# Kernel optimization log

Hardware: AMD Instinct MI355X
Metric: run time of the kernel (lower is better)

The kernel has to match this reference:

```python
import jax, jax.numpy as jnp
import numpy as np

N, D = 262144, 64
L, K = 4, 1024


def setup_inputs() -> dict:
    key = jax.random.key(0)
    k1, k2 = jax.random.split(key)
    features = jax.random.normal(k1, (N, D), dtype=jnp.float32)
    codebooks = jax.random.normal(k2, (L, K, D), dtype=jnp.float32)
    return {"features": features, "codebooks": codebooks}


def reference(features, codebooks):
    """Residual VQ: per level, nearest-center (L2) argmin, gather, subtract.

    Uses squared distances (same argmin as torch.cdist p=2).
    """

    def step(residuals, centers):
        # ||r - c||^2 = ||r||^2 - 2 r.c + ||c||^2   -> [N, K]
        d = (
            jnp.sum(residuals * residuals, axis=1, keepdims=True)
            - 2.0 * (residuals @ centers.T)
            + jnp.sum(centers * centers, axis=1)
        )
        idx = jnp.argmin(d, axis=1)          # [N] int32
        quantized = centers[idx]             # [N, D] gather
        return residuals - quantized, (quantized, idx)

    _, (quantized_levels, indices) = jax.lax.scan(step, features, codebooks)
    quantized_result = jnp.sum(quantized_levels, axis=0)  # sum over L levels
    return quantized_result, indices  # indices: [L, N]
```

## Files before the change

### kernel.cpp

```cpp
#include <hip/hip_runtime.h>
#include <math.h>

constexpr int RVQ_N = 262144;
constexpr int RVQ_D = 64;
constexpr int RVQ_L = 4;
constexpr int RVQ_K = 1024;

typedef __attribute__((ext_vector_type(8))) short short8;
typedef __attribute__((ext_vector_type(4))) float floatx4;

__device__ __forceinline__ unsigned short f2bf(float f) {
  unsigned int u = __float_as_uint(f);
  u += 0x7fffu + ((u >> 16) & 1u);
  return (unsigned short)(u >> 16);
}
__device__ __forceinline__ float bf2f(unsigned short h) {
  return __uint_as_float(((unsigned int)h) << 16);
}
__device__ __forceinline__ void split2(float x, unsigned short& h0,
                                       unsigned short& h1) {
  h0 = f2bf(x);
  float r1 = x - bf2f(h0);
  h1 = f2bf(r1);
}
__device__ __forceinline__ void load8(const float* p, float* v) {
  float4 a = *(const float4*)p;
  float4 b = *(const float4*)(p + 4);
  v[0] = a.x; v[1] = a.y; v[2] = a.z; v[3] = a.w;
  v[4] = b.x; v[5] = b.y; v[6] = b.z; v[7] = b.w;
}

__device__ __forceinline__ unsigned med3u(unsigned a, unsigned b, unsigned c) {
  unsigned d;
  asm("v_med3_u32 %0, %1, %2, %3" : "=v"(d) : "v"(a), "v"(b), "v"(c));
  return d;
}

__device__ __forceinline__ unsigned rowmin16(unsigned x) {
  unsigned y;
  y = (unsigned)__builtin_amdgcn_update_dpp(0, (int)x, 0x121, 0xF, 0xF, true);
  x = x < y ? x : y;
  y = (unsigned)__builtin_amdgcn_update_dpp(0, (int)x, 0x122, 0xF, 0xF, true);
  x = x < y ? x : y;
  y = (unsigned)__builtin_amdgcn_update_dpp(0, (int)x, 0x124, 0xF, 0xF, true);
  x = x < y ? x : y;
  y = (unsigned)__builtin_amdgcn_update_dpp(0, (int)x, 0x128, 0xF, 0xF, true);
  x = x < y ? x : y;
  return x;
}

__global__ __launch_bounds__(256) void rvq_prep_split(
    const float* __restrict__ cb, unsigned short* __restrict__ bh,
    unsigned short* __restrict__ bm) {
  int i = blockIdx.x * 256 + threadIdx.x;
  float c2 = -2.0f * cb[i];
  unsigned short h0, h1;
  split2(c2, h0, h1);
  bh[i] = h0;
  bm[i] = h1;
}

__global__ __launch_bounds__(256) void rvq_cnorm_kernel(
    const float* __restrict__ cb, float* __restrict__ cnorm,
    float* __restrict__ cnormB) {
  int i = blockIdx.x * blockDim.x + threadIdx.x;
  const float* c = cb + (size_t)i * RVQ_D;
  float a0 = 0.f, a1 = 0.f, a2 = 0.f, a3 = 0.f;
#pragma unroll
  for (int d = 0; d < RVQ_D; d += 4) {
    float4 v = *reinterpret_cast<const float4*>(c + d);
    a0 = fmaf(v.x, v.x, a0);
    a1 = fmaf(v.y, v.y, a1);
    a2 = fmaf(v.z, v.z, a2);
    a3 = fmaf(v.w, v.w, a3);
  }
  float s = (a0 + a1) + (a2 + a3);
  cnorm[i] = s;
  cnormB[i] = s + 256.0f;
}

__device__ __forceinline__ void load_bt(const unsigned short* __restrict__ bh,
                                        const unsigned short* __restrict__ bmp,
                                        const float* __restrict__ cnl, int nt,
                                        int m, int q, short8 (&b)[2][2],
                                        float& cc) {
  size_t rowoff = (size_t)(nt * 16 + m) * RVQ_D + q * 8;
  b[0][0] = *(const short8*)(bh + rowoff);
  b[0][1] = *(const short8*)(bh + rowoff + 32);
  b[1][0] = *(const short8*)(bmp + rowoff);
  b[1][1] = *(const short8*)(bmp + rowoff + 32);
  cc = cnl[nt * 16 + m];
}

__global__ __launch_bounds__(64, 3) void rvq_mfma_kernel(
    const float* __restrict__ feat, const float* __restrict__ cb,
    const unsigned short* __restrict__ cb_hi,
    const unsigned short* __restrict__ cb_mid,
    const float* __restrict__ cnorm, const float* __restrict__ cnormB,
    float* __restrict__ out_q, float* __restrict__ out_idx) {
  const int lane = threadIdx.x & 63;
  const int m = lane & 15;
  const int q = lane >> 4;
  const int base = blockIdx.x * 64;
  const int g = base + lane;

  int ci0 = 0, ci1 = 0, ci2 = 0;

  constexpr int AC[3] = {0, 0, 1};
  constexpr int BC[3] = {0, 1, 0};

#pragma unroll 1
  for (int l = 0; l < RVQ_L; ++l) {
    const unsigned short* bh = cb_hi + (size_t)l * RVQ_K * RVQ_D;
    const unsigned short* bmp = cb_mid + (size_t)l * RVQ_K * RVQ_D;
    const float* cnBl = cnormB + (size_t)l * RVQ_K;
    const float* cnl = cnorm + (size_t)l * RVQ_K;
    const float* cbl = cb + (size_t)l * RVQ_K * RVQ_D;

    short8 afr[4][2][2];
#pragma unroll
    for (int t = 0; t < 4; ++t) {
      const int p = t * 16 + m;
      int j0 = 0, j1 = 0, j2 = 0;
      if (l > 0) j0 = __shfl(ci0, p);
      if (l > 1) j1 = __shfl(ci1, p);
      if (l > 2) j2 = __shfl(ci2, p);
      const float* fp = feat + (size_t)(base + p) * RVQ_D;
      const float* c0p = cb + (size_t)j0 * RVQ_D;
      const float* c1p = cb + ((size_t)RVQ_K + j1) * RVQ_D;
      const float* c2p = cb + ((size_t)2 * RVQ_K + j2) * RVQ_D;
#pragma unroll
      for (int oct = 0; oct < 2; ++oct) {
        const int dof = oct * 32 + q * 8;
        float v[8];
        load8(fp + dof, v);
        if (l > 0) {
          float c[8];
          load8(c0p + dof, c);
#pragma unroll
          for (int e = 0; e < 8; ++e) v[e] -= c[e];
        }
        if (l > 1) {
          float c[8];
          load8(c1p + dof, c);
#pragma unroll
          for (int e = 0; e < 8; ++e) v[e] -= c[e];
        }
        if (l > 2) {
          float c[8];
          load8(c2p + dof, c);
#pragma unroll
          for (int e = 0; e < 8; ++e) v[e] -= c[e];
        }
#pragma unroll
        for (int e = 0; e < 8; ++e) {
          unsigned short h0, h1;
          split2(v[e], h0, h1);
          afr[t][0][oct][e] = (short)h0;
          afr[t][1][oct][e] = (short)h1;
        }
      }
    }

    unsigned p1[4][4], p2[4][4];
#pragma unroll
    for (int t = 0; t < 4; ++t)
#pragma unroll
      for (int r2 = 0; r2 < 4; ++r2) {
        p1[t][r2] = 0xFFFFFFFFu;
        p2[t][r2] = 0xFFFFFFFFu;
      }

    short8 bA[2][2], bB[2][2];
    float ccA, ccB;
    load_bt(bh, bmp, cnBl, 0, m, q, bA, ccA);

    for (int nt = 0; nt < RVQ_K / 16; nt += 2) {
      load_bt(bh, bmp, cnBl, nt + 1, m, q, bB, ccB);
      {
        floatx4 ccv;
        ccv[0] = ccA; ccv[1] = ccA; ccv[2] = ccA; ccv[3] = ccA;
        floatx4 acc[4];
        __builtin_amdgcn_s_setprio(1);
#pragma unroll
        for (int t = 0; t < 4; ++t) {
          floatx4 a = __builtin_amdgcn_mfma_f32_16x16x32_bf16(
              afr[t][AC[0]][0], bA[BC[0]][0], ccv, 0, 0, 0);
#pragma unroll
          for (int s = 0; s < 3; ++s)
#pragma unroll
            for (int oct = 0; oct < 2; ++oct) {
              if (s == 0 && oct == 0) continue;
              a = __builtin_amdgcn_mfma_f32_16x16x32_bf16(
                  afr[t][AC[s]][oct], bA[BC[s]][oct], a, 0, 0, 0);
            }
          acc[t] = a;
        }
        __builtin_amdgcn_s_setprio(0);
        unsigned nbits = (unsigned)nt;
#pragma unroll
        for (int t = 0; t < 4; ++t)
#pragma unroll
          for (int r2 = 0; r2 < 4; ++r2) {
            unsigned u = (__float_as_uint(acc[t][r2]) & 0xFFFFFFC0u) | nbits;
            p2[t][r2] = med3u(p1[t][r2], p2[t][r2], u);
            p1[t][r2] = p1[t][r2] < u ? p1[t][r2] : u;
          }
      }
      int ntn = (nt + 2 < RVQ_K / 16) ? nt + 2 : nt;
      load_bt(bh, bmp, cnBl, ntn, m, q, bA, ccA);
      {
        floatx4 ccv;
        ccv[0] = ccB; ccv[1] = ccB; ccv[2] = ccB; ccv[3] = ccB;
        floatx4 acc[4];
        __builtin_amdgcn_s_setprio(1);
#pragma unroll
        for (int t = 0; t < 4; ++t) {
          floatx4 a = __builtin_amdgcn_mfma_f32_16x16x32_bf16(
              afr[t][AC[0]][0], bB[BC[0]][0], ccv, 0, 0, 0);
#pragma unroll
          for (int s = 0; s < 3; ++s)
#pragma unroll
            for (int oct = 0; oct < 2; ++oct) {
              if (s == 0 && oct == 0) continue;
              a = __builtin_amdgcn_mfma_f32_16x16x32_bf16(
                  afr[t][AC[s]][oct], bB[BC[s]][oct], a, 0, 0, 0);
            }
          acc[t] = a;
        }
        __builtin_amdgcn_s_setprio(0);
        unsigned nbits = (unsigned)(nt + 1);
#pragma unroll
        for (int t = 0; t < 4; ++t)
#pragma unroll
          for (int r2 = 0; r2 < 4; ++r2) {
            unsigned u = (__float_as_uint(acc[t][r2]) & 0xFFFFFFC0u) | nbits;
            p2[t][r2] = med3u(p1[t][r2], p2[t][r2], u);
            p1[t][r2] = p1[t][r2] < u ? p1[t][r2] : u;
          }
      }
    }

    int cand[4] = {0, 0, 0, 0};
    const int srcl = ((lane >> 2) & 3) << 4;
#pragma unroll
    for (int t = 0; t < 4; ++t)
#pragma unroll
      for (int r2 = 0; r2 < 4; ++r2) {
        unsigned a = p1[t][r2], b = p2[t][r2];
        int ka = (int)((a & 63u) << 4) | m;
        int kb = (int)((b & 63u) << 4) | m;
        unsigned va = (a & 0xFFFFFC00u) | (unsigned)ka;
        unsigned vb = (b & 0xFFFFFC00u) | (unsigned)kb;
        if (vb < va) { unsigned tu = va; va = vb; vb = tu; }
        int ck[4];
#pragma unroll
        for (int pass = 0; pass < 4; ++pass) {
          unsigned gm = rowmin16(va);
          ck[pass] = (int)(gm & 1023u);
          bool hit = (va == gm);
          va = hit ? vb : va;
          vb = hit ? 0xFFFFFFFFu : vb;
        }
        int v1 = __shfl(ck[0], srcl);
        int v2 = __shfl(ck[1], srcl);
        int v3 = __shfl(ck[2], srcl);
        int v4 = __shfl(ck[3], srcl);
        bool take = (q == t) && ((lane & 3) == r2);
        if (take) { cand[0] = v1; cand[1] = v2; cand[2] = v3; cand[3] = v4; }
      }

    {
      int tmp;
      if (cand[0] > cand[1]) { tmp = cand[0]; cand[0] = cand[1]; cand[1] = tmp; }
      if (cand[2] > cand[3]) { tmp = cand[2]; cand[2] = cand[3]; cand[3] = tmp; }
      if (cand[0] > cand[2]) { tmp = cand[0]; cand[0] = cand[2]; cand[2] = tmp; }
      if (cand[1] > cand[3]) { tmp = cand[1]; cand[1] = cand[3]; cand[3] = tmp; }
      if (cand[1] > cand[2]) { tmp = cand[1]; cand[1] = cand[2]; cand[2] = tmp; }
    }

    float r_[RVQ_D];
    {
      const float4* f4p = (const float4*)(feat + (size_t)g * RVQ_D);
#pragma unroll
      for (int i = 0; i < 16; ++i) {
        float4 v = f4p[i];
        r_[4 * i + 0] = v.x; r_[4 * i + 1] = v.y;
        r_[4 * i + 2] = v.z; r_[4 * i + 3] = v.w;
      }
      if (l > 0) {
        const float4* cp = (const float4*)(cb + (size_t)ci0 * RVQ_D);
#pragma unroll
        for (int i = 0; i < 16; ++i) {
          float4 v = cp[i];
          r_[4 * i + 0] -= v.x; r_[4 * i + 1] -= v.y;
          r_[4 * i + 2] -= v.z; r_[4 * i + 3] -= v.w;
        }
      }
      if (l > 1) {
        const float4* cp = (const float4*)(cb + ((size_t)RVQ_K + ci1) * RVQ_D);
#pragma unroll
        for (int i = 0; i < 16; ++i) {
          float4 v = cp[i];
          r_[4 * i + 0] -= v.x; r_[4 * i + 1] -= v.y;
          r_[4 * i + 2] -= v.z; r_[4 * i + 3] -= v.w;
        }
      }
      if (l > 2) {
        const float4* cp =
            (const float4*)(cb + ((size_t)2 * RVQ_K + ci2) * RVQ_D);
#pragma unroll
        for (int i = 0; i < 16; ++i) {
          float4 v = cp[i];
          r_[4 * i + 0] -= v.x; r_[4 * i + 1] -= v.y;
          r_[4 * i + 2] -= v.z; r_[4 * i + 3] -= v.w;
        }
      }
    }

    float s0 = 0.f, s1 = 0.f, s2 = 0.f, s3 = 0.f;
#pragma unroll
    for (int i = 0; i < 16; ++i) {
      s0 = fmaf(r_[4 * i + 0], r_[4 * i + 0], s0);
      s1 = fmaf(r_[4 * i + 1], r_[4 * i + 1], s1);
      s2 = fmaf(r_[4 * i + 2], r_[4 * i + 2], s2);
      s3 = fmaf(r_[4 * i + 3], r_[4 * i + 3], s3);
    }
    const float rr = (s0 + s1) + (s2 + s3);

    float best = INFINITY;
    int ci = 0;
#pragma unroll
    for (int jc = 0; jc < 4; ++jc) {
      int k = cand[jc];
      const float4* c4 = (const float4*)(cbl + (size_t)k * RVQ_D);
      float a0 = 0.f, a1 = 0.f, a2 = 0.f, a3 = 0.f;
#pragma unroll
      for (int i = 0; i < 16; ++i) {
        float4 v = c4[i];
        a0 = fmaf(r_[4 * i + 0], v.x, a0);
        a1 = fmaf(r_[4 * i + 1], v.y, a1);
        a2 = fmaf(r_[4 * i + 2], v.z, a2);
        a3 = fmaf(r_[4 * i + 3], v.w, a3);
      }
      float dot = (a0 + a1) + (a2 + a3);
      float score = (rr - 2.0f * dot) + cnl[k];
      if (score < best) {
        best = score;
        ci = k;
      }
    }

    if (l == 0) ci0 = ci;
    else if (l == 1) ci1 = ci;
    else if (l == 2) ci2 = ci;

    if (l == RVQ_L - 1) {
      const float4* crow = (const float4*)(cbl + (size_t)ci * RVQ_D);
      const float4* f4p = (const float4*)(feat + (size_t)g * RVQ_D);
      float4* o4 = (float4*)(out_q + (size_t)g * RVQ_D);
#pragma unroll
      for (int i = 0; i < 16; ++i) {
        float4 cv = crow[i];
        float4 fv = f4p[i];
        float rn0 = r_[4 * i + 0] - cv.x;
        float rn1 = r_[4 * i + 1] - cv.y;
        float rn2 = r_[4 * i + 2] - cv.z;
        float rn3 = r_[4 * i + 3] - cv.w;
        float4 o;
        o.x = fv.x - rn0;
        o.y = fv.y - rn1;
        o.z = fv.z - rn2;
        o.w = fv.w - rn3;
        o4[i] = o;
      }
    }
    out_idx[(size_t)l * RVQ_N + g] = (float)ci;
  }
}

extern "C" void kernel_launch(void* const* d_in, const int* in_sizes, int n_in,
                              void* d_out, int out_size, void* d_ws,
                              size_t ws_size, hipStream_t stream) {
  const float* features = (const float*)d_in[0];
  const float* codebooks = (const float*)d_in[1];
  float* out_q = (float*)d_out;
  float* out_idx = (float*)d_out + (size_t)RVQ_N * RVQ_D;

  const size_t comp_elems = (size_t)RVQ_L * RVQ_K * RVQ_D;
  unsigned short* cb_hi = (unsigned short*)d_ws;
  unsigned short* cb_mid = cb_hi + comp_elems;
  float* cnorm = (float*)(cb_mid + comp_elems);
  float* cnormB = cnorm + (size_t)RVQ_L * RVQ_K;

  hipLaunchKernelGGL(rvq_prep_split, dim3(comp_elems / 256), dim3(256), 0,
                     stream, codebooks, cb_hi, cb_mid);
  hipLaunchKernelGGL(rvq_cnorm_kernel, dim3((RVQ_L * RVQ_K) / 256), dim3(256),
                     0, stream, codebooks, cnorm, cnormB);
  hipLaunchKernelGGL(rvq_mfma_kernel, dim3(RVQ_N / 64), dim3(64), 0, stream,
                     features, codebooks, cb_hi, cb_mid, cnorm, cnormB, out_q,
                     out_idx);
}
```

Measured before the change: 918.2 us.

## Stream codebook tiles through a 3-slot LDS ring via global_load_lds

Replaces the register double-buffered direct global loads of codebook tiles with a triple-buffered LDS ring filled by asynchronous global_load_lds instructions, prefetching three tiles ahead and waiting with vmcnt. The loop is de-unrolled to one tile per iteration. The aim is to hide global load latency and cut VGPR pressure from register staging. In exchange it adds LDS reads before every tile and relies on hand-written waitcnt ordering, where a wrong count or a slot being overwritten before it is read would give wrong results.

```diff
diff --git a/kernel.cpp b/kernel.cpp
--- a/kernel.cpp
+++ b/kernel.cpp
@@ -8,6 +8,11 @@
 
 typedef __attribute__((ext_vector_type(8))) short short8;
 typedef __attribute__((ext_vector_type(4))) float floatx4;
+
+#define GLOBAL_AS(p) ((const __attribute__((address_space(1))) unsigned int*)(p))
+#define LDS_AS(p) ((__attribute__((address_space(3))) unsigned int*)(p))
+
+constexpr unsigned SLOT_BYTES = 4352;
 
 __device__ __forceinline__ unsigned short f2bf(float f) {
   unsigned int u = __float_as_uint(f);
@@ -79,17 +84,21 @@
   cnormB[i] = s + 256.0f;
 }
 
-__device__ __forceinline__ void load_bt(const unsigned short* __restrict__ bh,
-                                        const unsigned short* __restrict__ bmp,
-                                        const float* __restrict__ cnl, int nt,
-                                        int m, int q, short8 (&b)[2][2],
-                                        float& cc) {
-  size_t rowoff = (size_t)(nt * 16 + m) * RVQ_D + q * 8;
-  b[0][0] = *(const short8*)(bh + rowoff);
-  b[0][1] = *(const short8*)(bh + rowoff + 32);
-  b[1][0] = *(const short8*)(bmp + rowoff);
-  b[1][1] = *(const short8*)(bmp + rowoff + 32);
-  cc = cnl[nt * 16 + m];
+__device__ __forceinline__ void stage_tile(
+    const unsigned short* __restrict__ bh,
+    const unsigned short* __restrict__ bmp, const float* __restrict__ cnl,
+    int tile, unsigned char* smem, unsigned so, int m, int q) {
+  const size_t re = (size_t)(tile * 16 + m) * RVQ_D + (size_t)q * 8;
+  unsigned char* s = smem + so;
+  __builtin_amdgcn_global_load_lds(GLOBAL_AS(bh + re), LDS_AS(s + 0), 16, 0, 0);
+  __builtin_amdgcn_global_load_lds(GLOBAL_AS(bh + re + 32), LDS_AS(s + 1024),
+                                   16, 0, 0);
+  __builtin_amdgcn_global_load_lds(GLOBAL_AS(bmp + re), LDS_AS(s + 2048), 16,
+                                   0, 0);
+  __builtin_amdgcn_global_load_lds(GLOBAL_AS(bmp + re + 32), LDS_AS(s + 3072),
+                                   16, 0, 0);
+  __builtin_amdgcn_global_load_lds(GLOBAL_AS(cnl + tile * 16 + m),
+                                   LDS_AS(s + 4096), 4, 0, 0);
 }
 
 __global__ __launch_bounds__(64, 3) void rvq_mfma_kernel(
@@ -98,6 +107,7 @@
     const unsigned short* __restrict__ cb_mid,
     const float* __restrict__ cnorm, const float* __restrict__ cnormB,
     float* __restrict__ out_q, float* __restrict__ out_idx) {
+  __shared__ __align__(16) unsigned char smem[3 * SLOT_BYTES];
   const int lane = threadIdx.x & 63;
   const int m = lane & 15;
   const int q = lane >> 4;
@@ -171,75 +181,56 @@
         p2[t][r2] = 0xFFFFFFFFu;
       }
 
-    short8 bA[2][2], bB[2][2];
-    float ccA, ccB;
-    load_bt(bh, bmp, cnBl, 0, m, q, bA, ccA);
-
-    for (int nt = 0; nt < RVQ_K / 16; nt += 2) {
-      load_bt(bh, bmp, cnBl, nt + 1, m, q, bB, ccB);
-      {
-        floatx4 ccv;
-        ccv[0] = ccA; ccv[1] = ccA; ccv[2] = ccA; ccv[3] = ccA;
-        floatx4 acc[4];
-        __builtin_amdgcn_s_setprio(1);
-#pragma unroll
-        for (int t = 0; t < 4; ++t) {
-          floatx4 a = __builtin_amdgcn_mfma_f32_16x16x32_bf16(
-              afr[t][AC[0]][0], bA[BC[0]][0], ccv, 0, 0, 0);
-#pragma unroll
-          for (int s = 0; s < 3; ++s)
-#pragma unroll
-            for (int oct = 0; oct < 2; ++oct) {
-              if (s == 0 && oct == 0) continue;
-              a = __builtin_amdgcn_mfma_f32_16x16x32_bf16(
-                  afr[t][AC[s]][oct], bA[BC[s]][oct], a, 0, 0, 0);
-            }
-          acc[t] = a;
-        }
-        __builtin_amdgcn_s_setprio(0);
-        unsigned nbits = (unsigned)nt;
-#pragma unroll
-        for (int t = 0; t < 4; ++t)
-#pragma unroll
-          for (int r2 = 0; r2 < 4; ++r2) {
-            unsigned u = (__float_as_uint(acc[t][r2]) & 0xFFFFFFC0u) | nbits;
-            p2[t][r2] = med3u(p1[t][r2], p2[t][r2], u);
-            p1[t][r2] = p1[t][r2] < u ? p1[t][r2] : u;
+    stage_tile(bh, bmp, cnBl, 0, smem, 0 * SLOT_BYTES, m, q);
+    stage_tile(bh, bmp, cnBl, 1, smem, 1 * SLOT_BYTES, m, q);
+    stage_tile(bh, bmp, cnBl, 2, smem, 2 * SLOT_BYTES, m, q);
+
+    unsigned so = 0;
+#pragma unroll 1
+    for (int nt = 0; nt < RVQ_K / 16; ++nt) {
+      asm volatile("s_waitcnt vmcnt(10)" ::: "memory");
+      const unsigned char* s = smem + so;
+      short8 bb[2][2];
+      bb[0][0] = *(const short8*)(s + (size_t)lane * 16);
+      bb[0][1] = *(const short8*)(s + 1024 + (size_t)lane * 16);
+      bb[1][0] = *(const short8*)(s + 2048 + (size_t)lane * 16);
+      bb[1][1] = *(const short8*)(s + 3072 + (size_t)lane * 16);
+      float cc = *(const float*)(s + 4096 + (size_t)lane * 4);
+
+      floatx4 ccv;
+      ccv[0] = cc; ccv[1] = cc; ccv[2] = cc; ccv[3] = cc;
+      floatx4 acc[4];
+      __builtin_amdgcn_s_setprio(1);
+#pragma unroll
+      for (int t = 0; t < 4; ++t) {
+        floatx4 a = __builtin_amdgcn_mfma_f32_16x16x32_bf16(
+            afr[t][AC[0]][0], bb[BC[0]][0], ccv, 0, 0, 0);
+#pragma unroll
+        for (int ss = 0; ss < 3; ++ss)
+#pragma unroll
+          for (int oct = 0; oct < 2; ++oct) {
+            if (ss == 0 && oct == 0) continue;
+            a = __builtin_amdgcn_mfma_f32_16x16x32_bf16(
+                afr[t][AC[ss]][oct], bb[BC[ss]][oct], a, 0, 0, 0);
           }
-      }
-      int ntn = (nt + 2 < RVQ_K / 16) ? nt + 2 : nt;
-      load_bt(bh, bmp, cnBl, ntn, m, q, bA, ccA);
-      {
-        floatx4 ccv;
-        ccv[0] = ccB; ccv[1] = ccB; ccv[2] = ccB; ccv[3] = ccB;
-        floatx4 acc[4];
-        __builtin_amdgcn_s_setprio(1);
-#pragma unroll
-        for (int t = 0; t < 4; ++t) {
-          floatx4 a = __builtin_amdgcn_mfma_f32_16x16x32_bf16(
-              afr[t][AC[0]][0], bB[BC[0]][0], ccv, 0, 0, 0);
-#pragma unroll
-          for (int s = 0; s < 3; ++s)
-#pragma unroll
-            for (int oct = 0; oct < 2; ++oct) {
-              if (s == 0 && oct == 0) continue;
-              a = __builtin_amdgcn_mfma_f32_16x16x32_bf16(
-                  afr[t][AC[s]][oct], bB[BC[s]][oct], a, 0, 0, 0);
-            }
-          acc[t] = a;
-        }
-        __builtin_amdgcn_s_setprio(0);
-        unsigned nbits = (unsigned)(nt + 1);
-#pragma unroll
-        for (int t = 0; t < 4; ++t)
-#pragma unroll
-          for (int r2 = 0; r2 < 4; ++r2) {
-            unsigned u = (__float_as_uint(acc[t][r2]) & 0xFFFFFFC0u) | nbits;
-            p2[t][r2] = med3u(p1[t][r2], p2[t][r2], u);
-            p1[t][r2] = p1[t][r2] < u ? p1[t][r2] : u;
-          }
-      }
-    }
+        acc[t] = a;
+      }
+      __builtin_amdgcn_s_setprio(0);
+      unsigned nbits = (unsigned)nt;
+#pragma unroll
+      for (int t = 0; t < 4; ++t)
+#pragma unroll
+        for (int r2 = 0; r2 < 4; ++r2) {
+          unsigned u = (__float_as_uint(acc[t][r2]) & 0xFFFFFFC0u) | nbits;
+          p2[t][r2] = med3u(p1[t][r2], p2[t][r2], u);
+          p1[t][r2] = p1[t][r2] < u ? p1[t][r2] : u;
+        }
+
+      int tgt = (nt + 3 < RVQ_K / 16) ? nt + 3 : (RVQ_K / 16 - 1);
+      stage_tile(bh, bmp, cnBl, tgt, smem, so, m, q);
+      so = (so == 2 * SLOT_BYTES) ? 0u : so + SLOT_BYTES;
+    }
+    asm volatile("s_waitcnt vmcnt(0)" ::: "memory");
 
     int cand[4] = {0, 0, 0, 0};
     const int srcl = ((lane >> 2) & 3) << 4;
```

New measurement: 1.041 ms. 1.13x slower.
